# Optimization experiments

Hardware: AMD Instinct MI355X
Metric: run time of the kernel (lower is better)

## Reference

```python
import jax, jax.numpy as jnp
import numpy as np

# Production-scale dims (RecSys CTR): huge batch, modest feature dim -> memory-bound.
BATCH = 262144
DIM = 128
NUM_DOMAIN = 8
EPS = 1e-3  # Keras BatchNormalization default epsilon


def setup_inputs() -> dict:
    key = jax.random.key(0)
    k1, k2 = jax.random.split(key)
    inputs = jax.random.normal(k1, (BATCH, DIM), dtype=jnp.float32)
    domain_index = jax.random.randint(k2, (BATCH,), 0, NUM_DOMAIN, dtype=jnp.int32)
    # Learned params, matching Constant(0.5)/Zeros initializers in build().
    global_gamma = jnp.full((DIM,), 0.5, dtype=jnp.float32)
    global_beta = jnp.zeros((DIM,), dtype=jnp.float32)
    domain_gamma = jnp.full((NUM_DOMAIN, DIM), 0.5, dtype=jnp.float32)
    domain_beta = jnp.zeros((NUM_DOMAIN, DIM), dtype=jnp.float32)
    return {
        "inputs": inputs,
        "global_gamma": global_gamma,
        "global_beta": global_beta,
        "domain_gamma": domain_gamma,
        "domain_beta": domain_beta,
        "domain_index": domain_index,
    }


def reference(inputs, global_gamma, global_beta, domain_gamma, domain_beta, domain_index):
    """Partitioned Normalization (training-mode BN stats per domain).

    Equivalent to the per-domain loop of boolean_mask -> BatchNorm(center=False,
    scale=False) -> affine -> scatter, but expressed as one segmented reduction
    plus gathers (every row belongs to exactly one domain, so the scatter is a
    full per-row update).
    """
    seg = domain_index  # [B] int, values in [0, NUM_DOMAIN)
    ones = jnp.ones((inputs.shape[0],), dtype=inputs.dtype)
    counts = jax.ops.segment_sum(ones, seg, num_segments=NUM_DOMAIN)        # [K]
    sums = jax.ops.segment_sum(inputs, seg, num_segments=NUM_DOMAIN)        # [K, D]
    sqsums = jax.ops.segment_sum(inputs * inputs, seg, num_segments=NUM_DOMAIN)  # [K, D]
    n = jnp.maximum(counts, 1.0)[:, None]  # guard empty domains (their stats are unused)
    mean = sums / n                                        # [K, D] per-domain mean
    var = jnp.maximum(sqsums / n - mean * mean, 0.0)       # biased variance, as Keras BN
    # Normalize each row with its own domain's statistics (gather [B, D]).
    x_norm = (inputs - mean[seg]) * jax.lax.rsqrt(var[seg] + EPS)
    gamma = global_gamma + domain_gamma[seg]               # [B, D]
    beta = global_beta + domain_beta[seg]                  # [B, D]
    return gamma * x_norm + beta
```

## Files before the change

### kernel.cpp

```cpp
#include <hip/hip_runtime.h>
#include <hip/hip_bf16.h>


#define DIM 128
#define NDOM 8
#define PENT (NDOM + 2 * NDOM * DIM)
#define EPSV 1e-3f
#define WREG 2048

__global__ __launch_bounds__(256) void pn_reduce(const float4* __restrict__ x4,
                                                 const int* __restrict__ seg,
                                                 float* __restrict__ partials,
                                                 int rowsPerBlock) {
  __shared__ float acc[8 * WREG];
  __shared__ float lcnt[NDOM];
  const int tid = threadIdx.x;
  const int w = tid >> 6;
  const int l = tid & 63;
  const int h = l >> 5;
  const int g = l & 31;
  float* reg = acc + (w * 2 + h) * WREG;

  for (int i = tid; i < 2 * WREG; i += 256) ((float4*)acc)[i] = make_float4(0.f, 0.f, 0.f, 0.f);
  if (tid < NDOM) lcnt[tid] = 0.f;
  __syncthreads();

  const int rowsPerWave = rowsPerBlock >> 2;
  const int row0 = blockIdx.x * rowsPerBlock + w * rowsPerWave;

#define RMW(S, V)                                    \
  {                                                  \
    float* bs = reg + (S) * 128 + g * 4;             \
    float* bq = bs + NDOM * DIM;                     \
    float4 os = *(float4*)bs;                        \
    float4 oq = *(float4*)bq;                        \
    os.x += (V).x;                                   \
    os.y += (V).y;                                   \
    os.z += (V).z;                                   \
    os.w += (V).w;                                   \
    oq.x = fmaf((V).x, (V).x, oq.x);                 \
    oq.y = fmaf((V).y, (V).y, oq.y);                 \
    oq.z = fmaf((V).z, (V).z, oq.z);                 \
    oq.w = fmaf((V).w, (V).w, oq.w);                 \
    *(float4*)bs = os;                               \
    *(float4*)bq = oq;                               \
  }

  for (int it = 0; it < rowsPerWave; it += 8) {
    const int r = row0 + it;
    const int4 sgA = *(const int4*)(seg + r);
    const int4 sgB = *(const int4*)(seg + r + 4);
    const float4 v0 = x4[(size_t)(r + 0 + h) * 32 + g];
    const float4 v1 = x4[(size_t)(r + 2 + h) * 32 + g];
    const float4 v2 = x4[(size_t)(r + 4 + h) * 32 + g];
    const float4 v3 = x4[(size_t)(r + 6 + h) * 32 + g];
    const int s0 = h ? sgA.y : sgA.x;
    const int s1 = h ? sgA.w : sgA.z;
    const int s2 = h ? sgB.y : sgB.x;
    const int s3 = h ? sgB.w : sgB.z;
    RMW(s0, v0)
    RMW(s1, v1)
    RMW(s2, v2)
    RMW(s3, v3)
  }
#undef RMW
  __syncthreads();

  for (int i = tid; i < rowsPerBlock; i += 256)
    atomicAdd(&lcnt[seg[blockIdx.x * rowsPerBlock + i]], 1.f);
  __syncthreads();

  float* outp = partials + (size_t)blockIdx.x * PENT;
  if (tid < NDOM) outp[tid] = lcnt[tid];
  for (int i = tid; i < 2 * NDOM * DIM; i += 256) {
    float v = 0.f;
#pragma unroll
    for (int rr = 0; rr < 8; ++rr) v += acc[rr * WREG + i];
    outp[NDOM + i] = v;
  }
}

__global__ __launch_bounds__(256) void pn_reduce2(const float* __restrict__ partials,
                                                  float* __restrict__ partials2,
                                                  int NB) {
  const int b = blockIdx.x;
  const int per = NB >> 6;
  const int b0 = b * per;
  const int tid = threadIdx.x;
  float acc[9];
#pragma unroll
  for (int i = 0; i < 9; ++i) acc[i] = 0.f;
  for (int j = b0; j < b0 + per; ++j) {
    const float* p = partials + (size_t)j * PENT;
#pragma unroll
    for (int i = 0; i < 9; ++i) {
      const int e = tid + i * 256;
      if (e < PENT) acc[i] += p[e];
    }
  }
  float* o = partials2 + (size_t)b * PENT;
#pragma unroll
  for (int i = 0; i < 9; ++i) {
    const int e = tid + i * 256;
    if (e < PENT) o[e] = acc[i];
  }
}

__global__ __launch_bounds__(256) void pn_finalize(const float* __restrict__ partials2,
                                                   const float* __restrict__ gg,
                                                   const float* __restrict__ gb,
                                                   const float* __restrict__ dg,
                                                   const float* __restrict__ db,
                                                   float* __restrict__ stats) {
  const int t = blockIdx.x * 256 + threadIdx.x;
  const int k = t >> 7;
  const int d = t & (DIM - 1);
  float c = 0.f, s = 0.f, q = 0.f;
  for (int j = 0; j < 64; ++j) {
    const float* p = partials2 + (size_t)j * PENT;
    c += p[k];
    s += p[NDOM + t];
    q += p[NDOM + NDOM * DIM + t];
  }
  const float n = fmaxf(c, 1.f);
  const float mean = s / n;
  const float var = fmaxf(q / n - mean * mean, 0.f);
  const float rstd = rsqrtf(var + EPSV);
  const float scale = (gg[d] + dg[t]) * rstd;
  const float shift = (gb[d] + db[t]) - scale * mean;
  stats[t] = scale;
  stats[NDOM * DIM + t] = shift;
}

__global__ __launch_bounds__(256) void pn_apply(const float* __restrict__ x,
                                                const int* __restrict__ seg,
                                                const float* __restrict__ stats,
                                                float* __restrict__ out) {
  const int g = blockIdx.x * 256 + threadIdx.x;
  const int row = g >> 5;
  const int c4 = g & 31;
  const int s = seg[row];
  const float4 xv = ((const float4*)x)[g];
  const float4 a = ((const float4*)(stats + s * DIM))[c4];
  const float4 b = ((const float4*)(stats + NDOM * DIM + s * DIM))[c4];
  float4 o;
  o.x = fmaf(xv.x, a.x, b.x);
  o.y = fmaf(xv.y, a.y, b.y);
  o.z = fmaf(xv.z, a.z, b.z);
  o.w = fmaf(xv.w, a.w, b.w);
  ((float4*)out)[g] = o;
}

extern "C" void kernel_launch(void* const* d_in, const int* in_sizes, int n_in,
                              void* d_out, int out_size, void* d_ws, size_t ws_size,
                              hipStream_t stream) {
  const float* x = (const float*)d_in[0];
  const float* gg = (const float*)d_in[1];
  const float* gb = (const float*)d_in[2];
  const float* dg = (const float*)d_in[3];
  const float* db = (const float*)d_in[4];
  const int* seg = (const int*)d_in[5];
  float* out = (float*)d_out;

  const int B = in_sizes[5];

  int NB = 1024;
  while (NB > 64 &&
         ((size_t)NB * PENT + 64 * PENT + 2 * NDOM * DIM) * sizeof(float) > ws_size)
    NB >>= 1;
  float* partials = (float*)d_ws;
  float* partials2 = partials + (size_t)NB * PENT;
  float* stats = partials2 + (size_t)64 * PENT;

  const int rpb = B / NB;

  pn_reduce<<<NB, 256, 0, stream>>>((const float4*)x, seg, partials, rpb);
  pn_reduce2<<<64, 256, 0, stream>>>(partials, partials2, NB);
  pn_finalize<<<4, 256, 0, stream>>>(partials2, gg, gb, dg, db, stats);

  const int nblk = (B * (DIM / 4)) / 256;
  pn_apply<<<nblk, 256, 0, stream>>>(x, seg, stats, out);
}
```

Baseline: 101.0 us.

## Fuse reduce, finalize and apply into one cooperative persistent kernel

Replaces the four separate launches (partial reduce, second-level reduce, finalize, apply) with a single cooperative kernel that uses grid-wide syncs between phases. The grid is sized from occupancy and CU count so each block owns a contiguous row chunk, and it applies the normalization to the same rows it reduced, which may let part of x be re-read from cache. It removes launch gaps between kernels, but it adds grid.sync barriers, leaves most blocks idle during the small reduce and finalize phases, and uses fewer blocks for the apply pass. The old multi-kernel path is kept as a fallback if the cooperative launch fails.

```diff
diff --git a/kernel.cpp b/kernel.cpp
--- a/kernel.cpp
+++ b/kernel.cpp
@@ -1,5 +1,8 @@
 #include <hip/hip_runtime.h>
 #include <hip/hip_bf16.h>
+#include <hip/hip_cooperative_groups.h>
+
+namespace cg = cooperative_groups;
 
 
 #define DIM 128
@@ -8,25 +11,32 @@
 #define EPSV 1e-3f
 #define WREG 2048
 
-__global__ __launch_bounds__(256) void pn_reduce(const float4* __restrict__ x4,
-                                                 const int* __restrict__ seg,
-                                                 float* __restrict__ partials,
-                                                 int rowsPerBlock) {
+__global__ __launch_bounds__(256) void pn_fused(
+    const float4* __restrict__ x4, const int* __restrict__ seg,
+    const float* __restrict__ gg, const float* __restrict__ gb,
+    const float* __restrict__ dg, const float* __restrict__ db,
+    float* __restrict__ partials, float* __restrict__ partials2,
+    float* __restrict__ stats, float4* __restrict__ out, int B) {
+  cg::grid_group grid = cg::this_grid();
   __shared__ float acc[8 * WREG];
   __shared__ float lcnt[NDOM];
   const int tid = threadIdx.x;
+  const int NBLK = gridDim.x;
+  const int chunk = B / NBLK;
+  const int row0blk = blockIdx.x * chunk;
   const int w = tid >> 6;
   const int l = tid & 63;
   const int h = l >> 5;
   const int g = l & 31;
   float* reg = acc + (w * 2 + h) * WREG;
 
-  for (int i = tid; i < 2 * WREG; i += 256) ((float4*)acc)[i] = make_float4(0.f, 0.f, 0.f, 0.f);
+  for (int i = tid; i < 2 * WREG; i += 256)
+    ((float4*)acc)[i] = make_float4(0.f, 0.f, 0.f, 0.f);
   if (tid < NDOM) lcnt[tid] = 0.f;
   __syncthreads();
 
-  const int rowsPerWave = rowsPerBlock >> 2;
-  const int row0 = blockIdx.x * rowsPerBlock + w * rowsPerWave;
+  const int rowsPerWave = chunk >> 2;
+  const int row0 = row0blk + w * rowsPerWave;
 
 #define RMW(S, V)                                    \
   {                                                  \
@@ -45,7 +55,6 @@
     *(float4*)bs = os;                               \
     *(float4*)bq = oq;                               \
   }
-
   for (int it = 0; it < rowsPerWave; it += 8) {
     const int r = row0 + it;
     const int4 sgA = *(const int4*)(seg + r);
@@ -66,10 +75,143 @@
 #undef RMW
   __syncthreads();
 
+  for (int i = tid; i < chunk; i += 256)
+    atomicAdd(&lcnt[seg[row0blk + i]], 1.f);
+  __syncthreads();
+
+  {
+    float* outp = partials + (size_t)blockIdx.x * PENT;
+    if (tid < NDOM) outp[tid] = lcnt[tid];
+    for (int i = tid; i < 2 * NDOM * DIM; i += 256) {
+      float v = 0.f;
+#pragma unroll
+      for (int rr = 0; rr < 8; ++rr) v += acc[rr * WREG + i];
+      outp[NDOM + i] = v;
+    }
+  }
+  grid.sync();
+
+  if (blockIdx.x < 64) {
+    const int per = NBLK >> 6;
+    const int b0 = blockIdx.x * per;
+    float a2[9];
+#pragma unroll
+    for (int i = 0; i < 9; ++i) a2[i] = 0.f;
+    for (int j = b0; j < b0 + per; ++j) {
+      const float* p = partials + (size_t)j * PENT;
+#pragma unroll
+      for (int i = 0; i < 9; ++i) {
+        const int e = tid + i * 256;
+        if (e < PENT) a2[i] += p[e];
+      }
+    }
+    float* o = partials2 + (size_t)blockIdx.x * PENT;
+#pragma unroll
+    for (int i = 0; i < 9; ++i) {
+      const int e = tid + i * 256;
+      if (e < PENT) o[e] = a2[i];
+    }
+  }
+  grid.sync();
+
+  if (blockIdx.x < 4) {
+    const int t = blockIdx.x * 256 + tid;
+    const int k = t >> 7;
+    const int d = t & (DIM - 1);
+    float c = 0.f, s = 0.f, q = 0.f;
+    for (int j = 0; j < 64; ++j) {
+      const float* p = partials2 + (size_t)j * PENT;
+      c += p[k];
+      s += p[NDOM + t];
+      q += p[NDOM + NDOM * DIM + t];
+    }
+    const float n = fmaxf(c, 1.f);
+    const float mean = s / n;
+    const float var = fmaxf(q / n - mean * mean, 0.f);
+    const float rstd = rsqrtf(var + EPSV);
+    const float scale = (gg[d] + dg[t]) * rstd;
+    const float shift = (gb[d] + db[t]) - scale * mean;
+    stats[t] = scale;
+    stats[NDOM * DIM + t] = shift;
+  }
+  grid.sync();
+
+  {
+    const int f40 = row0blk * 32;
+    const int nf4 = chunk * 32;
+#pragma unroll 4
+    for (int i = tid; i < nf4; i += 256) {
+      const int gi = f40 + i;
+      const int row = gi >> 5;
+      const int c4 = gi & 31;
+      const int s = seg[row];
+      const float4 xv = x4[gi];
+      const float4 a = ((const float4*)(stats + s * DIM))[c4];
+      const float4 b = ((const float4*)(stats + NDOM * DIM + s * DIM))[c4];
+      float4 o;
+      o.x = fmaf(xv.x, a.x, b.x);
+      o.y = fmaf(xv.y, a.y, b.y);
+      o.z = fmaf(xv.z, a.z, b.z);
+      o.w = fmaf(xv.w, a.w, b.w);
+      out[gi] = o;
+    }
+  }
+}
+
+__global__ __launch_bounds__(256) void pn_reduce(const float4* __restrict__ x4,
+                                                 const int* __restrict__ seg,
+                                                 float* __restrict__ partials,
+                                                 int rowsPerBlock) {
+  __shared__ float acc[8 * WREG];
+  __shared__ float lcnt[NDOM];
+  const int tid = threadIdx.x;
+  const int w = tid >> 6;
+  const int l = tid & 63;
+  const int h = l >> 5;
+  const int g = l & 31;
+  float* reg = acc + (w * 2 + h) * WREG;
+
+  for (int i = tid; i < 2 * WREG; i += 256)
+    ((float4*)acc)[i] = make_float4(0.f, 0.f, 0.f, 0.f);
+  if (tid < NDOM) lcnt[tid] = 0.f;
+  __syncthreads();
+
+  const int rowsPerWave = rowsPerBlock >> 2;
+  const int row0 = blockIdx.x * rowsPerBlock + w * rowsPerWave;
+
+#define RMW(S, V)                                    \
+  {                                                  \
+    float* bs = reg + (S) * 128 + g * 4;             \
+    float* bq = bs + NDOM * DIM;                     \
+    float4 os = *(float4*)bs;                        \
+    float4 oq = *(float4*)bq;                        \
+    os.x += (V).x; os.y += (V).y; os.z += (V).z; os.w += (V).w; \
+    oq.x = fmaf((V).x, (V).x, oq.x);                 \
+    oq.y = fmaf((V).y, (V).y, oq.y);                 \
+    oq.z = fmaf((V).z, (V).z, oq.z);                 \
+    oq.w = fmaf((V).w, (V).w, oq.w);                 \
+    *(float4*)bs = os;                               \
+    *(float4*)bq = oq;                               \
+  }
+  for (int it = 0; it < rowsPerWave; it += 8) {
+    const int r = row0 + it;
+    const int4 sgA = *(const int4*)(seg + r);
+    const int4 sgB = *(const int4*)(seg + r + 4);
+    const float4 v0 = x4[(size_t)(r + 0 + h) * 32 + g];
+    const float4 v1 = x4[(size_t)(r + 2 + h) * 32 + g];
+    const float4 v2 = x4[(size_t)(r + 4 + h) * 32 + g];
+    const float4 v3 = x4[(size_t)(r + 6 + h) * 32 + g];
+    const int s0 = h ? sgA.y : sgA.x;
+    const int s1 = h ? sgA.w : sgA.z;
+    const int s2 = h ? sgB.y : sgB.x;
+    const int s3 = h ? sgB.w : sgB.z;
+    RMW(s0, v0) RMW(s1, v1) RMW(s2, v2) RMW(s3, v3)
+  }
+#undef RMW
+  __syncthreads();
   for (int i = tid; i < rowsPerBlock; i += 256)
     atomicAdd(&lcnt[seg[blockIdx.x * rowsPerBlock + i]], 1.f);
   __syncthreads();
-
   float* outp = partials + (size_t)blockIdx.x * PENT;
   if (tid < NDOM) outp[tid] = lcnt[tid];
   for (int i = tid; i < 2 * NDOM * DIM; i += 256) {
@@ -161,23 +303,41 @@
   const float* db = (const float*)d_in[4];
   const int* seg = (const int*)d_in[5];
   float* out = (float*)d_out;
-
-  const int B = in_sizes[5];
-
-  int NB = 1024;
-  while (NB > 64 &&
-         ((size_t)NB * PENT + 64 * PENT + 2 * NDOM * DIM) * sizeof(float) > ws_size)
-    NB >>= 1;
+  int B = in_sizes[5];
+
+  int occ = 2, ncu = 256;
+  (void)hipOccupancyMaxActiveBlocksPerMultiprocessor(&occ, (const void*)pn_fused, 256, 0);
+  if (occ < 1) occ = 1;
+  if (occ > 2) occ = 2;
+  int dev = 0;
+  (void)hipGetDevice(&dev);
+  (void)hipDeviceGetAttribute(&ncu, hipDeviceAttributeMultiprocessorCount, dev);
+  if (ncu <= 0) ncu = 256;
+  int nblk = occ * ncu;
+  while (B % (nblk * 4) != 0) nblk >>= 1;
+  if (nblk < 64) nblk = 64;
+
   float* partials = (float*)d_ws;
-  float* partials2 = partials + (size_t)NB * PENT;
+  float* partials2 = partials + (size_t)nblk * PENT;
   float* stats = partials2 + (size_t)64 * PENT;
 
-  const int rpb = B / NB;
-
-  pn_reduce<<<NB, 256, 0, stream>>>((const float4*)x, seg, partials, rpb);
-  pn_reduce2<<<64, 256, 0, stream>>>(partials, partials2, NB);
-  pn_finalize<<<4, 256, 0, stream>>>(partials2, gg, gb, dg, db, stats);
-
-  const int nblk = (B * (DIM / 4)) / 256;
-  pn_apply<<<nblk, 256, 0, stream>>>(x, seg, stats, out);
-}
+  const float4* x4 = (const float4*)x;
+  float4* out4 = (float4*)out;
+  void* args[] = {(void*)&x4, (void*)&seg, (void*)&gg, (void*)&gb, (void*)&dg,
+                  (void*)&db, (void*)&partials, (void*)&partials2, (void*)&stats,
+                  (void*)&out4, (void*)&B};
+  hipError_t err = hipLaunchCooperativeKernel((void*)pn_fused, dim3(nblk),
+                                              dim3(256), args, 0, stream);
+  if (err != hipSuccess) {
+    int NB = 1024;
+    float* p1 = (float*)d_ws;
+    float* p2 = p1 + (size_t)NB * PENT;
+    float* st = p2 + (size_t)64 * PENT;
+    const int rpb = B / NB;
+    pn_reduce<<<NB, 256, 0, stream>>>((const float4*)x, seg, p1, rpb);
+    pn_reduce2<<<64, 256, 0, stream>>>(p1, p2, NB);
+    pn_finalize<<<4, 256, 0, stream>>>(p2, gg, gb, dg, db, st);
+    const int nblk2 = (B * (DIM / 4)) / 256;
+    pn_apply<<<nblk2, 256, 0, stream>>>(x, seg, st, out);
+  }
+}
```

Result: slower. 174.8 us (+73.1%).
